# Optimization experiments

Measured on AMD Instinct MI355X. Metric: run time of the kernel, lower is better.

Reference implementation:

```python
import jax, jax.numpy as jnp
import numpy as np


def _spmm(rows, cols, vals, h, n):
    # sparse_dense_matmul(A, h) with A in COO form: out[r] += val * h[c]
    return jax.ops.segment_sum(vals[:, None] * h[cols], rows, num_segments=n)


def setup_inputs() -> dict:
    key = jax.random.key(0)
    ks = jax.random.split(key, 8)
    N, Din, Dout, D, E = 50000, 256, 128, 8, 800000
    x = jax.random.normal(ks[0], (N, Din), jnp.float32)
    h = jax.random.normal(ks[1], (N, Dout), jnp.float32)
    rows = jax.random.randint(ks[2], (D, E), 0, N, dtype=jnp.int32)
    cols = jax.random.randint(ks[3], (D, E), 0, N, dtype=jnp.int32)
    vals = jax.random.uniform(ks[4], (D, E), jnp.float32)
    W = jax.random.normal(ks[5], (Din, Dout), jnp.float32) * 0.05
    V = jax.random.normal(ks[6], (Dout, Dout), jnp.float32) * 0.05
    alpha = jax.random.normal(ks[7], (D, 1), jnp.float32)
    return dict(x=x, h=h, rows=rows, cols=cols, vals=vals, W=W, V=V, alpha=alpha)


def reference(x, h, rows, cols, vals, W, V, alpha):
    N = x.shape[0]
    D = rows.shape[0]
    # h1 = x @ W (x is tf.SparseTensor in the original; same math densely)
    h1 = x @ W
    # per-device: (A_d @ h) @ V  -> [D, N, Dout]; loop over small fixed device set
    h2 = jnp.stack([_spmm(rows[d], cols[d], vals[d], h, N) @ V for d in range(D)])
    # tf.nn.softmax on [D,1] normalizes the size-1 last axis -> all ones (faithful)
    w = jax.nn.softmax(alpha, axis=-1)[:, 0]  # [D]
    comb = jnp.einsum('dno,d->no', h2, w)  # matches reshape/transpose/matmul combine
    return jax.nn.relu(h1 + comb)
```

## Files before the change

kernel.cpp:

```cpp
#include <hip/hip_runtime.h>
#include <hip/hip_bf16.h>

#define DOUT 128
#define DIN  256
#define BROWS 64
#define MAXNB 1024
#define BIN_CHUNK 4096
#define SCHUNK 9216

typedef __attribute__((ext_vector_type(8))) short bf16x8;
typedef __attribute__((ext_vector_type(4))) float f32x4;
union FragU { uint4 q; bf16x8 f; };

static __device__ __forceinline__ float bf16lo_to_f(unsigned u) {
    return __uint_as_float(u << 16);
}
static __device__ __forceinline__ float bf16hi_to_f(unsigned u) {
    return __uint_as_float(u & 0xffff0000u);
}
static __device__ __forceinline__ unsigned f_to_bf16_bits(float f) {
    unsigned u = __float_as_uint(f);
    return (u + 0x7fffu + ((u >> 16) & 1u)) >> 16;
}
static __device__ __forceinline__ unsigned pack2(float a, float b) {
    return f_to_bf16_bits(a) | (f_to_bf16_bits(b) << 16);
}

__global__ __launch_bounds__(256) void conv_wv(const float* __restrict__ W,
                                               const float* __restrict__ V,
                                               unsigned short* __restrict__ WT,
                                               unsigned short* __restrict__ VT) {
    int n = blockIdx.x;
    int t = threadIdx.x;
    WT[n * 256 + t] = (unsigned short)f_to_bf16_bits(W[t * DOUT + n]);
    if (t < 128) VT[n * 128 + t] = (unsigned short)f_to_bf16_bits(V[t * DOUT + n]);
}

__global__ __launch_bounds__(256) void hv_gemm(const float* __restrict__ h,
                                               const unsigned* __restrict__ VTu,
                                               unsigned short* __restrict__ hV,
                                               int N) {
    __shared__ unsigned xs[64 * 20];
    int t = threadIdx.x;
    int r0 = blockIdx.x * 64;
    int w = t >> 6, l = t & 63;
    int wm = w >> 1, wn = w & 1;
    int lm = l & 15, lk = l >> 4;
    f32x4 acc[2][4];
#pragma unroll
    for (int i = 0; i < 2; ++i)
#pragma unroll
        for (int j = 0; j < 4; ++j) acc[i][j] = (f32x4){0.f, 0.f, 0.f, 0.f};

    int srow = min(r0 + (t >> 2), N - 1);
    const float* hrow = h + (size_t)srow * DOUT + (t & 3) * 8;
    unsigned* xsw = &xs[(t >> 2) * 20 + (t & 3) * 4];

    for (int k0 = 0; k0 < DOUT; k0 += 32) {
        float4 f0 = *(const float4*)(hrow + k0);
        float4 f1 = *(const float4*)(hrow + k0 + 4);
        ((uint4*)xsw)[0] = make_uint4(pack2(f0.x, f0.y), pack2(f0.z, f0.w),
                                      pack2(f1.x, f1.y), pack2(f1.z, f1.w));
        __syncthreads();
        FragU a[2], b[4];
#pragma unroll
        for (int i = 0; i < 2; ++i)
            a[i].q = *(const uint4*)&xs[(wm * 32 + i * 16 + lm) * 20 + lk * 4];
#pragma unroll
        for (int j = 0; j < 4; ++j)
            b[j].q = *(const uint4*)(VTu + (size_t)(wn * 64 + j * 16 + lm) * 64 +
                                     (k0 >> 1) + lk * 4);
#pragma unroll
        for (int i = 0; i < 2; ++i)
#pragma unroll
            for (int j = 0; j < 4; ++j)
                acc[i][j] = __builtin_amdgcn_mfma_f32_16x16x32_bf16(
                    a[i].f, b[j].f, acc[i][j], 0, 0, 0);
        __syncthreads();
    }
#pragma unroll
    for (int i = 0; i < 2; ++i)
#pragma unroll
        for (int j = 0; j < 4; ++j) {
            int gr0 = r0 + wm * 32 + i * 16 + lk * 4;
            int gc = wn * 64 + j * 16 + lm;
#pragma unroll
            for (int r = 0; r < 4; ++r) {
                int gr = gr0 + r;
                if (gr < N)
                    hV[(size_t)gr * DOUT + gc] =
                        (unsigned short)f_to_bf16_bits(acc[i][j][r]);
            }
        }
}

__global__ void bucket_hist(const int* __restrict__ rows, int* __restrict__ gcnt,
                            int nE, int nb) {
    __shared__ int hc[MAXNB];
    for (int i = threadIdx.x; i < nb; i += blockDim.x) hc[i] = 0;
    __syncthreads();
    for (int i = blockIdx.x * blockDim.x + threadIdx.x; i < nE;
         i += gridDim.x * blockDim.x)
        atomicAdd(&hc[rows[i] / BROWS], 1);
    __syncthreads();
    for (int i = threadIdx.x; i < nb; i += blockDim.x)
        if (hc[i]) atomicAdd(&gcnt[i], hc[i]);
}

__global__ __launch_bounds__(1024) void scan_buckets(const int* __restrict__ gcnt,
                                                     int* __restrict__ bptr,
                                                     int* __restrict__ gcur, int nb) {
    __shared__ int sbuf[MAXNB];
    int t = threadIdx.x;
    int c = (t < nb) ? gcnt[t] : 0;
    sbuf[t] = c;
    __syncthreads();
    for (int off = 1; off < 1024; off <<= 1) {
        int v = (t >= off) ? sbuf[t - off] : 0;
        __syncthreads();
        sbuf[t] += v;
        __syncthreads();
    }
    if (t == 0) bptr[0] = 0;
    if (t < nb) { bptr[t + 1] = sbuf[t]; gcur[t] = sbuf[t] - c; }
}

__global__ __launch_bounds__(1024) void bin_edges(const int* __restrict__ rows,
                                                  const int* __restrict__ cols,
                                                  const float* __restrict__ vals,
                                                  int* __restrict__ gcur,
                                                  unsigned* __restrict__ ecv4,
                                                  unsigned char* __restrict__ erow,
                                                  int nE, int nb) {
    __shared__ unsigned secv[BIN_CHUNK];
    __shared__ unsigned short srow16[BIN_CHUNK];
    __shared__ int hcnt[MAXNB], sbuf[MAXNB], loff[MAXNB], lcur[MAXNB], gbase[MAXNB];
    int t = threadIdx.x;
    int base = blockIdx.x * BIN_CHUNK;
    int nvalid = min(BIN_CHUNK, nE - base);
    hcnt[t] = 0;
    __syncthreads();
    for (int j = t; j < nvalid; j += 1024)
        atomicAdd(&hcnt[rows[base + j] / BROWS], 1);
    __syncthreads();
    int myc = hcnt[t];
    sbuf[t] = myc;
    __syncthreads();
    for (int off = 1; off < 1024; off <<= 1) {
        int v = (t >= off) ? sbuf[t - off] : 0;
        __syncthreads();
        sbuf[t] += v;
        __syncthreads();
    }
    int excl = sbuf[t] - myc;
    loff[t] = excl;
    lcur[t] = excl;
    if (t < nb && myc > 0) gbase[t] = atomicAdd(&gcur[t], myc);
    __syncthreads();
    for (int j = t; j < nvalid; j += 1024) {
        int i = base + j;
        unsigned r = (unsigned)rows[i];
        int bk = (int)r / BROWS;
        int slot = atomicAdd(&lcur[bk], 1);
        secv[slot] = ((unsigned)cols[i] << 16) | f_to_bf16_bits(vals[i]);
        srow16[slot] = (unsigned short)r;
    }
    __syncthreads();
    for (int j = t; j < nvalid; j += 1024) {
        unsigned r = srow16[j];
        int bk = (int)r / BROWS;
        int dst = gbase[bk] + (j - loff[bk]);
        ecv4[dst] = secv[j];
        erow[dst] = (unsigned char)(r & (BROWS - 1));
    }
}

__global__ __launch_bounds__(512) void spmm_sorted(const int* __restrict__ bptr,
                                                   const unsigned* __restrict__ ecv4,
                                                   const unsigned char* __restrict__ erow,
                                                   const unsigned* __restrict__ hV,
                                                   float* __restrict__ out, int N) {
    __shared__ __align__(16) unsigned srec[SCHUNK + BROWS * 8];
    __shared__ int rcnt[BROWS], sbuf[BROWS], rptr[BROWS + 1], rcur[BROWS];
    int t = threadIdx.x;
    int b = blockIdx.x;
    int wave = t >> 6, lane = t & 63;
    int hf = lane >> 5;
    int cl = lane & 31;
    int beg = bptr[b], end = bptr[b + 1];
    const uint2* hv2 = (const uint2*)hV;

    float4 acc[8];
#pragma unroll
    for (int j = 0; j < 8; ++j) acc[j] = make_float4(0.f, 0.f, 0.f, 0.f);

    for (int cb = beg; cb < end; cb += SCHUNK) {
        int nval = min(SCHUNK, end - cb);
        if (t < BROWS) rcnt[t] = 0;
        __syncthreads();
        for (int j = t; j < nval; j += 512)
            atomicAdd(&rcnt[erow[cb + j]], 1);
        __syncthreads();
        int c = (t < BROWS) ? rcnt[t] : 0;
        int cp = (c + 7) & ~7;
        if (t < BROWS) sbuf[t] = cp;
        __syncthreads();
        for (int off = 1; off < BROWS; off <<= 1) {
            int add = (t < BROWS && t >= off) ? sbuf[t - off] : 0;
            __syncthreads();
            if (t < BROWS) sbuf[t] += add;
            __syncthreads();
        }
        if (t == 0) rptr[0] = 0;
        if (t < BROWS) { rptr[t + 1] = sbuf[t]; rcur[t] = sbuf[t] - cp; }
        __syncthreads();
        for (int j = t; j < nval; j += 512) {
            int rloc = erow[cb + j];
            int slot = atomicAdd(&rcur[rloc], 1);
            srec[slot] = ecv4[cb + j];
        }
        __syncthreads();
        if (t < BROWS) {
            int e0 = rcur[t];
            int e1 = rptr[t + 1];
            for (int k = e0; k < e1; ++k) srec[k] = 0u;
        }
        __syncthreads();
#pragma unroll
        for (int rr = 0; rr < 8; ++rr) {
            int rloc = wave * 8 + rr;
            int s = rptr[rloc];
            int ng = (rptr[rloc + 1] - s) >> 3;
            const uint4* sp = (const uint4*)&srec[s + 4 * hf];
            float4 a = acc[rr];
            for (int g = 0; g < ng; ++g) {
                uint4 q = sp[2 * g];
                uint2 u0 = hv2[((q.x >> 16) << 5) | cl];
                uint2 u1 = hv2[((q.y >> 16) << 5) | cl];
                uint2 u2 = hv2[((q.z >> 16) << 5) | cl];
                uint2 u3 = hv2[((q.w >> 16) << 5) | cl];
                float v0 = bf16lo_to_f(q.x);
                float v1 = bf16lo_to_f(q.y);
                float v2 = bf16lo_to_f(q.z);
                float v3 = bf16lo_to_f(q.w);
                a.x += v0 * bf16lo_to_f(u0.x); a.y += v0 * bf16hi_to_f(u0.x);
                a.z += v0 * bf16lo_to_f(u0.y); a.w += v0 * bf16hi_to_f(u0.y);
                a.x += v1 * bf16lo_to_f(u1.x); a.y += v1 * bf16hi_to_f(u1.x);
                a.z += v1 * bf16lo_to_f(u1.y); a.w += v1 * bf16hi_to_f(u1.y);
                a.x += v2 * bf16lo_to_f(u2.x); a.y += v2 * bf16hi_to_f(u2.x);
                a.z += v2 * bf16lo_to_f(u2.y); a.w += v2 * bf16hi_to_f(u2.y);
                a.x += v3 * bf16lo_to_f(u3.x); a.y += v3 * bf16hi_to_f(u3.x);
                a.z += v3 * bf16lo_to_f(u3.y); a.w += v3 * bf16hi_to_f(u3.y);
            }
            acc[rr] = a;
        }
        __syncthreads();
    }
#pragma unroll
    for (int rr = 0; rr < 8; ++rr) {
        float4 a = acc[rr];
        a.x += __shfl_xor(a.x, 32);
        a.y += __shfl_xor(a.y, 32);
        a.z += __shfl_xor(a.z, 32);
        a.w += __shfl_xor(a.w, 32);
        int gr = b * BROWS + wave * 8 + rr;
        if (hf == 0 && gr < N)
            ((float4*)(out + (size_t)gr * DOUT))[cl] = a;
    }
}

__global__ __launch_bounds__(256) void epi_xw(const float* __restrict__ x,
                                              const unsigned* __restrict__ WTu,
                                              float* __restrict__ out, int N) {
    __shared__ unsigned xs[64 * 20];
    int t = threadIdx.x;
    int r0 = blockIdx.x * 64;
    int w = t >> 6, l = t & 63;
    int wm = w >> 1, wn = w & 1;
    int lm = l & 15, lk = l >> 4;
    f32x4 acc[2][4];
#pragma unroll
    for (int i = 0; i < 2; ++i)
#pragma unroll
        for (int j = 0; j < 4; ++j) acc[i][j] = (f32x4){0.f, 0.f, 0.f, 0.f};

    int srow = min(r0 + (t >> 2), N - 1);
    const float* xrow = x + (size_t)srow * DIN + (t & 3) * 8;
    unsigned* xsw = &xs[(t >> 2) * 20 + (t & 3) * 4];

    for (int k0 = 0; k0 < DIN; k0 += 32) {
        float4 f0 = *(const float4*)(xrow + k0);
        float4 f1 = *(const float4*)(xrow + k0 + 4);
        ((uint4*)xsw)[0] = make_uint4(pack2(f0.x, f0.y), pack2(f0.z, f0.w),
                                      pack2(f1.x, f1.y), pack2(f1.z, f1.w));
        __syncthreads();
        FragU a[2], b[4];
#pragma unroll
        for (int i = 0; i < 2; ++i)
            a[i].q = *(const uint4*)&xs[(wm * 32 + i * 16 + lm) * 20 + lk * 4];
#pragma unroll
        for (int j = 0; j < 4; ++j)
            b[j].q = *(const uint4*)(WTu + (size_t)(wn * 64 + j * 16 + lm) * 128 +
                                     (k0 >> 1) + lk * 4);
#pragma unroll
        for (int i = 0; i < 2; ++i)
#pragma unroll
            for (int j = 0; j < 4; ++j)
                acc[i][j] = __builtin_amdgcn_mfma_f32_16x16x32_bf16(
                    a[i].f, b[j].f, acc[i][j], 0, 0, 0);
        __syncthreads();
    }
#pragma unroll
    for (int i = 0; i < 2; ++i)
#pragma unroll
        for (int j = 0; j < 4; ++j) {
            int gr0 = r0 + wm * 32 + i * 16 + lk * 4;
            int gc = wn * 64 + j * 16 + lm;
#pragma unroll
            for (int r = 0; r < 4; ++r) {
                int gr = gr0 + r;
                if (gr < N) {
                    size_t o = (size_t)gr * DOUT + gc;
                    out[o] = fmaxf(acc[i][j][r] + out[o], 0.f);
                }
            }
        }
}

__global__ void spmm_atomic(const int* __restrict__ rows,
                            const int* __restrict__ cols,
                            const float* __restrict__ vals,
                            const float* __restrict__ h,
                            float* __restrict__ S, int nEdges) {
    int wave = (int)((blockIdx.x * blockDim.x + threadIdx.x) >> 6);
    int lane = threadIdx.x & 63;
    if (wave >= nEdges) return;
    int r = rows[wave], c = cols[wave];
    float v = vals[wave];
    float2 hv = ((const float2*)(h + (size_t)c * DOUT))[lane];
    float* srow = S + (size_t)r * DOUT;
    atomicAdd(srow + 2 * lane,     v * hv.x);
    atomicAdd(srow + 2 * lane + 1, v * hv.y);
}

__global__ __launch_bounds__(256) void fused_out_full(const float* __restrict__ x,
                                                      const float* __restrict__ W,
                                                      const float* __restrict__ V,
                                                      float* __restrict__ out, int N) {
    __shared__ float xs[DIN];
    __shared__ float ss[DOUT];
    int r = blockIdx.x;
    int col = threadIdx.x & 127;
    if (threadIdx.x < 128) {
        float2 xv = ((const float2*)(x + (size_t)r * DIN))[col];
        xs[2 * col] = xv.x; xs[2 * col + 1] = xv.y;
        ss[col] = out[(size_t)r * DOUT + col];
    }
    __syncthreads();
    if (threadIdx.x >= 128) return;
    float acc = 0.f;
    for (int k = 0; k < DIN; ++k) acc += xs[k] * W[k * DOUT + col];
    for (int k = 0; k < DOUT; ++k) acc += ss[k] * V[k * DOUT + col];
    out[(size_t)r * DOUT + col] = fmaxf(acc, 0.f);
}

static inline size_t align256(size_t v) { return (v + 255) & ~(size_t)255; }

extern "C" void kernel_launch(void* const* d_in, const int* in_sizes, int n_in,
                              void* d_out, int out_size, void* d_ws, size_t ws_size,
                              hipStream_t stream) {
    const float* x    = (const float*)d_in[0];
    const float* h    = (const float*)d_in[1];
    const int*   rows = (const int*)d_in[2];
    const int*   cols = (const int*)d_in[3];
    const float* vals = (const float*)d_in[4];
    const float* W    = (const float*)d_in[5];
    const float* V    = (const float*)d_in[6];

    int nE = in_sizes[2];
    int N  = in_sizes[1] / DOUT;
    int nb = (N + BROWS - 1) / BROWS;
    float* out = (float*)d_out;

    size_t o_hV   = 0;
    size_t o_WT   = o_hV   + align256((size_t)N * DOUT * 2);
    size_t o_VT   = o_WT   + align256((size_t)128 * 256 * 2);
    size_t o_gcnt = o_VT   + align256((size_t)128 * 128 * 2);
    size_t o_bptr = o_gcnt + align256((size_t)nb * 4);
    size_t o_gcur = o_bptr + align256((size_t)(nb + 1) * 4);
    size_t o_ecv4 = o_gcur + align256((size_t)nb * 4);
    size_t o_erow = o_ecv4 + align256((size_t)nE * 4);
    size_t need   = o_erow + (size_t)nE;

    if (ws_size >= need && N < 65536 && nb <= MAXNB) {
        char* p = (char*)d_ws;
        unsigned short* hV = (unsigned short*)(p + o_hV);
        unsigned short* WT = (unsigned short*)(p + o_WT);
        unsigned short* VT = (unsigned short*)(p + o_VT);
        int*      gcnt = (int*)(p + o_gcnt);
        int*      bptr = (int*)(p + o_bptr);
        int*      gcur = (int*)(p + o_gcur);
        unsigned* ecv4 = (unsigned*)(p + o_ecv4);
        unsigned char* erow = (unsigned char*)(p + o_erow);

        conv_wv<<<128, 256, 0, stream>>>(W, V, WT, VT);
        hv_gemm<<<(N + 63) / 64, 256, 0, stream>>>(h, (const unsigned*)VT, hV, N);
        hipMemsetAsync(gcnt, 0, (size_t)nb * 4, stream);
        bucket_hist<<<1024, 256, 0, stream>>>(rows, gcnt, nE, nb);
        scan_buckets<<<1, 1024, 0, stream>>>(gcnt, bptr, gcur, nb);
        bin_edges<<<(nE + BIN_CHUNK - 1) / BIN_CHUNK, 1024, 0, stream>>>(
            rows, cols, vals, gcur, ecv4, erow, nE, nb);
        spmm_sorted<<<nb, 512, 0, stream>>>(bptr, ecv4, erow,
                                            (const unsigned*)hV, out, N);
        epi_xw<<<(N + 63) / 64, 256, 0, stream>>>(x, (const unsigned*)WT, out, N);
    } else {
        hipMemsetAsync(out, 0, (size_t)N * DOUT * 4, stream);
        spmm_atomic<<<(nE + 3) / 4, 256, 0, stream>>>(rows, cols, vals, h, out, nE);
        fused_out_full<<<N, 128, 0, stream>>>(x, W, V, out, N);
    }
}
```

Baseline: 499.2 us.

## Fuse x@W epilogue into sorted SpMM kernel and use wave-shuffle scans

Merges the separate epi_xw kernel into the sorted SpMM kernel. The SpMM row results are staged in shared memory, then the same block computes the x@W tile with MFMA and writes relu(sum) straight to out. This removes one launch and the write-then-read of the 25 MB output. It also replaces the shared-memory Hillis-Steele scans in scan_buckets, bin_edges and the per-chunk row scan with wave-level shuffle scans, cutting barriers. The price is a longer-running SpMM block with 8 waves doing the smaller GEMM tile, plus extra shared-memory reuse.

```diff
diff --git a/kernel.cpp b/kernel.cpp
--- a/kernel.cpp
+++ b/kernel.cpp
@@ -110,19 +110,30 @@
 __global__ __launch_bounds__(1024) void scan_buckets(const int* __restrict__ gcnt,
                                                      int* __restrict__ bptr,
                                                      int* __restrict__ gcur, int nb) {
-    __shared__ int sbuf[MAXNB];
+    __shared__ int wtot[16];
     int t = threadIdx.x;
     int c = (t < nb) ? gcnt[t] : 0;
-    sbuf[t] = c;
-    __syncthreads();
-    for (int off = 1; off < 1024; off <<= 1) {
-        int v = (t >= off) ? sbuf[t - off] : 0;
-        __syncthreads();
-        sbuf[t] += v;
-        __syncthreads();
-    }
+    int v = c;
+#pragma unroll
+    for (int d = 1; d < 64; d <<= 1) {
+        int u = __shfl_up(v, d);
+        if ((t & 63) >= d) v += u;
+    }
+    if ((t & 63) == 63) wtot[t >> 6] = v;
+    __syncthreads();
+    if (t < 16) {
+        int wv = wtot[t];
+#pragma unroll
+        for (int d = 1; d < 16; d <<= 1) {
+            int u = __shfl_up(wv, d);
+            if (t >= d) wv += u;
+        }
+        wtot[t] = wv;
+    }
+    __syncthreads();
+    int incl = v + ((t >= 64) ? wtot[(t >> 6) - 1] : 0);
     if (t == 0) bptr[0] = 0;
-    if (t < nb) { bptr[t + 1] = sbuf[t]; gcur[t] = sbuf[t] - c; }
+    if (t < nb) { bptr[t + 1] = incl; gcur[t] = incl - c; }
 }
 
 __global__ __launch_bounds__(1024) void bin_edges(const int* __restrict__ rows,
@@ -134,7 +145,8 @@
                                                   int nE, int nb) {
     __shared__ unsigned secv[BIN_CHUNK];
     __shared__ unsigned short srow16[BIN_CHUNK];
-    __shared__ int hcnt[MAXNB], sbuf[MAXNB], loff[MAXNB], lcur[MAXNB], gbase[MAXNB];
+    __shared__ int hcnt[MAXNB], loff[MAXNB], lcur[MAXNB], gbase[MAXNB];
+    __shared__ int wtot[16];
     int t = threadIdx.x;
     int base = blockIdx.x * BIN_CHUNK;
     int nvalid = min(BIN_CHUNK, nE - base);
@@ -144,15 +156,25 @@
         atomicAdd(&hcnt[rows[base + j] / BROWS], 1);
     __syncthreads();
     int myc = hcnt[t];
-    sbuf[t] = myc;
-    __syncthreads();
-    for (int off = 1; off < 1024; off <<= 1) {
-        int v = (t >= off) ? sbuf[t - off] : 0;
-        __syncthreads();
-        sbuf[t] += v;
-        __syncthreads();
-    }
-    int excl = sbuf[t] - myc;
+    int v = myc;
+#pragma unroll
+    for (int d = 1; d < 64; d <<= 1) {
+        int u = __shfl_up(v, d);
+        if ((t & 63) >= d) v += u;
+    }
+    if ((t & 63) == 63) wtot[t >> 6] = v;
+    __syncthreads();
+    if (t < 16) {
+        int wv = wtot[t];
+#pragma unroll
+        for (int d = 1; d < 16; d <<= 1) {
+            int u = __shfl_up(wv, d);
+            if (t >= d) wv += u;
+        }
+        wtot[t] = wv;
+    }
+    __syncthreads();
+    int excl = v - myc + ((t >= 64) ? wtot[(t >> 6) - 1] : 0);
     loff[t] = excl;
     lcur[t] = excl;
     if (t < nb && myc > 0) gbase[t] = atomicAdd(&gcur[t], myc);
@@ -175,13 +197,15 @@
     }
 }
 
-__global__ __launch_bounds__(512) void spmm_sorted(const int* __restrict__ bptr,
-                                                   const unsigned* __restrict__ ecv4,
-                                                   const unsigned char* __restrict__ erow,
-                                                   const unsigned* __restrict__ hV,
-                                                   float* __restrict__ out, int N) {
+__global__ __launch_bounds__(512) void spmm_epi(const int* __restrict__ bptr,
+                                                const unsigned* __restrict__ ecv4,
+                                                const unsigned char* __restrict__ erow,
+                                                const unsigned* __restrict__ hV,
+                                                const float* __restrict__ x,
+                                                const unsigned* __restrict__ WTu,
+                                                float* __restrict__ out, int N) {
     __shared__ __align__(16) unsigned srec[SCHUNK + BROWS * 8];
-    __shared__ int rcnt[BROWS], sbuf[BROWS], rptr[BROWS + 1], rcur[BROWS];
+    __shared__ int rcnt[BROWS], rptr[BROWS + 1], rcur[BROWS];
     int t = threadIdx.x;
     int b = blockIdx.x;
     int wave = t >> 6, lane = t & 63;
@@ -201,18 +225,19 @@
         for (int j = t; j < nval; j += 512)
             atomicAdd(&rcnt[erow[cb + j]], 1);
         __syncthreads();
-        int c = (t < BROWS) ? rcnt[t] : 0;
-        int cp = (c + 7) & ~7;
-        if (t < BROWS) sbuf[t] = cp;
-        __syncthreads();
-        for (int off = 1; off < BROWS; off <<= 1) {
-            int add = (t < BROWS && t >= off) ? sbuf[t - off] : 0;
-            __syncthreads();
-            if (t < BROWS) sbuf[t] += add;
-            __syncthreads();
-        }
-        if (t == 0) rptr[0] = 0;
-        if (t < BROWS) { rptr[t + 1] = sbuf[t]; rcur[t] = sbuf[t] - cp; }
+        if (wave == 0) {
+            int c = rcnt[lane];
+            int cp = (c + 7) & ~7;
+            int v = cp;
+#pragma unroll
+            for (int d = 1; d < 64; d <<= 1) {
+                int u = __shfl_up(v, d);
+                if (lane >= d) v += u;
+            }
+            rptr[lane + 1] = v;
+            rcur[lane] = v - cp;
+            if (lane == 0) rptr[0] = 0;
+        }
         __syncthreads();
         for (int j = t; j < nval; j += 512) {
             int rloc = erow[cb + j];
@@ -256,6 +281,8 @@
         }
         __syncthreads();
     }
+
+    float* Sbuf = (float*)srec;
 #pragma unroll
     for (int rr = 0; rr < 8; ++rr) {
         float4 a = acc[rr];
@@ -263,68 +290,52 @@
         a.y += __shfl_xor(a.y, 32);
         a.z += __shfl_xor(a.z, 32);
         a.w += __shfl_xor(a.w, 32);
-        int gr = b * BROWS + wave * 8 + rr;
-        if (hf == 0 && gr < N)
-            ((float4*)(out + (size_t)gr * DOUT))[cl] = a;
-    }
-}
-
-__global__ __launch_bounds__(256) void epi_xw(const float* __restrict__ x,
-                                              const unsigned* __restrict__ WTu,
-                                              float* __restrict__ out, int N) {
-    __shared__ unsigned xs[64 * 20];
-    int t = threadIdx.x;
-    int r0 = blockIdx.x * 64;
-    int w = t >> 6, l = t & 63;
-    int wm = w >> 1, wn = w & 1;
-    int lm = l & 15, lk = l >> 4;
-    f32x4 acc[2][4];
-#pragma unroll
-    for (int i = 0; i < 2; ++i)
-#pragma unroll
-        for (int j = 0; j < 4; ++j) acc[i][j] = (f32x4){0.f, 0.f, 0.f, 0.f};
-
-    int srow = min(r0 + (t >> 2), N - 1);
-    const float* xrow = x + (size_t)srow * DIN + (t & 3) * 8;
-    unsigned* xsw = &xs[(t >> 2) * 20 + (t & 3) * 4];
+        if (hf == 0)
+            *(float4*)&Sbuf[(wave * 8 + rr) * 132 + 4 * cl] = a;
+    }
+    __syncthreads();
+
+    unsigned* xs = srec + 64 * 132;
+    int wm = wave >> 1, wn = wave & 1;
+    int lm = lane & 15, lk = lane >> 4;
+    f32x4 acc4[4];
+#pragma unroll
+    for (int j = 0; j < 4; ++j) acc4[j] = (f32x4){0.f, 0.f, 0.f, 0.f};
+
+    int r0 = b * BROWS;
+    int srow = min(r0 + (t >> 3), N - 1);
+    const float* xrow = x + (size_t)srow * DIN + (t & 7) * 4;
+    unsigned* xsw = &xs[(t >> 3) * 18 + (t & 7) * 2];
 
     for (int k0 = 0; k0 < DIN; k0 += 32) {
-        float4 f0 = *(const float4*)(xrow + k0);
-        float4 f1 = *(const float4*)(xrow + k0 + 4);
-        ((uint4*)xsw)[0] = make_uint4(pack2(f0.x, f0.y), pack2(f0.z, f0.w),
-                                      pack2(f1.x, f1.y), pack2(f1.z, f1.w));
-        __syncthreads();
-        FragU a[2], b[4];
-#pragma unroll
-        for (int i = 0; i < 2; ++i)
-            a[i].q = *(const uint4*)&xs[(wm * 32 + i * 16 + lm) * 20 + lk * 4];
-#pragma unroll
-        for (int j = 0; j < 4; ++j)
-            b[j].q = *(const uint4*)(WTu + (size_t)(wn * 64 + j * 16 + lm) * 128 +
-                                     (k0 >> 1) + lk * 4);
-#pragma unroll
-        for (int i = 0; i < 2; ++i)
-#pragma unroll
-            for (int j = 0; j < 4; ++j)
-                acc[i][j] = __builtin_amdgcn_mfma_f32_16x16x32_bf16(
-                    a[i].f, b[j].f, acc[i][j], 0, 0, 0);
-        __syncthreads();
-    }
-#pragma unroll
-    for (int i = 0; i < 2; ++i)
+        float4 f = *(const float4*)(xrow + k0);
+        xsw[0] = pack2(f.x, f.y);
+        xsw[1] = pack2(f.z, f.w);
+        __syncthreads();
+        FragU a;
+        a.q = *(const uint4*)&xs[(wm * 16 + lm) * 18 + lk * 4];
 #pragma unroll
         for (int j = 0; j < 4; ++j) {
-            int gr0 = r0 + wm * 32 + i * 16 + lk * 4;
-            int gc = wn * 64 + j * 16 + lm;
-#pragma unroll
-            for (int r = 0; r < 4; ++r) {
-                int gr = gr0 + r;
-                if (gr < N) {
-                    size_t o = (size_t)gr * DOUT + gc;
-                    out[o] = fmaxf(acc[i][j][r] + out[o], 0.f);
-                }
-            }
-        }
+            FragU bb;
+            bb.q = *(const uint4*)(WTu + (size_t)(wn * 64 + j * 16 + lm) * 128 +
+                                   (k0 >> 1) + lk * 4);
+            acc4[j] = __builtin_amdgcn_mfma_f32_16x16x32_bf16(
+                a.f, bb.f, acc4[j], 0, 0, 0);
+        }
+        __syncthreads();
+    }
+#pragma unroll
+    for (int j = 0; j < 4; ++j) {
+        int gc = wn * 64 + j * 16 + lm;
+#pragma unroll
+        for (int r = 0; r < 4; ++r) {
+            int lr = wm * 16 + 4 * lk + r;
+            int gr = r0 + lr;
+            if (gr < N)
+                out[(size_t)gr * DOUT + gc] =
+                    fmaxf(acc4[j][r] + Sbuf[lr * 132 + gc], 0.f);
+        }
+    }
 }
 
 __global__ void spmm_atomic(const int* __restrict__ rows,
@@ -410,9 +421,8 @@
         scan_buckets<<<1, 1024, 0, stream>>>(gcnt, bptr, gcur, nb);
         bin_edges<<<(nE + BIN_CHUNK - 1) / BIN_CHUNK, 1024, 0, stream>>>(
             rows, cols, vals, gcur, ecv4, erow, nE, nb);
-        spmm_sorted<<<nb, 512, 0, stream>>>(bptr, ecv4, erow,
-                                            (const unsigned*)hV, out, N);
-        epi_xw<<<(N + 63) / 64, 256, 0, stream>>>(x, (const unsigned*)WT, out, N);
+        spmm_epi<<<nb, 512, 0, stream>>>(bptr, ecv4, erow, (const unsigned*)hV,
+                                         x, (const unsigned*)WT, out, N);
     } else {
         hipMemsetAsync(out, 0, (size_t)N * DOUT * 4, stream);
         spmm_atomic<<<(nE + 3) / 4, 256, 0, stream>>>(rows, cols, vals, h, out, nE);
```

Result: no change. 491.3 us (-1.6%).
